# Optimization experiments

Measured on AMD Instinct MI355X. Metric: run time of the kernel, lower is better.

Reference implementation:

```python
import jax, jax.numpy as jnp
import numpy as np

# ---- ATSSPostProcessor config ----
PRE_NMS_THRESH = 0.05
PRE_NMS_TOP_N  = 400      # k candidates per image (pre_nms_top_n)
NMS_THRESH     = 0.4
POST_TOP_N     = 100      # fpn_post_nms_top_n
MIN_SIZE       = 0.0
NUM_ANGLE_BINS = 90
BBOX_W         = (10.0, 10.0, 5.0, 5.0)   # box_coder xywh weights; angle is passthrough (argmax-90 deg)
N, C, H, W     = 4, 15, 256, 256           # A=1 anchor per location
STRIDE, ANCHOR_SIZE = 8.0, 64.0
MAXV = 16                                   # vertex buffer for quad-quad clipping


def setup_inputs():
    key = jax.random.key(0)
    k1, k2, k3, k4 = jax.random.split(key, 4)
    box_cls = jax.random.normal(k1, (N, C, H, W), jnp.float32) - 2.0  # sigmoid ~0.12 avg -> plenty of candidates
    box_regression = jax.random.normal(k2, (N, 4, H, W), jnp.float32) * 0.5
    centerness = jax.random.normal(k3, (N, 1, H, W), jnp.float32)
    angle = jax.random.normal(k4, (N, NUM_ANGLE_BINS, H, W), jnp.float32)
    # xywha anchors on the stride-8 grid, row-major (H, W) to match permute_and_flatten ordering
    ys, xs = jnp.meshgrid(jnp.arange(H, dtype=jnp.float32), jnp.arange(W, dtype=jnp.float32), indexing='ij')
    cx = (xs.reshape(-1) + 0.5) * STRIDE
    cy = (ys.reshape(-1) + 0.5) * STRIDE
    wh = jnp.full((H * W,), ANCHOR_SIZE, jnp.float32)
    a0 = jnp.zeros((H * W,), jnp.float32)
    anchors = jnp.broadcast_to(jnp.stack([cx, cy, wh, wh, a0], -1), (N, H * W, 5))
    return {"box_cls": box_cls, "box_regression": box_regression, "centerness": centerness,
            "angle": angle, "anchors": jnp.asarray(anchors)}


def xywha_to_corners(b):
    # b [..., 5] (cx,cy,w,h,angle_deg) -> [..., 4, 2], CCW order
    cx, cy, w, h, a = b[..., 0], b[..., 1], b[..., 2], b[..., 3], b[..., 4]
    t = a * (jnp.pi / 180.0)
    c, s = jnp.cos(t), jnp.sin(t)
    ox = jnp.asarray([1., -1., -1., 1.], b.dtype) * (w[..., None] * 0.5)
    oy = jnp.asarray([1., 1., -1., -1.], b.dtype) * (h[..., None] * 0.5)
    x = cx[..., None] + ox * c[..., None] - oy * s[..., None]
    y = cy[..., None] + ox * s[..., None] + oy * c[..., None]
    return jnp.stack([x, y], -1)


def _clip_edge(poly, n, p1, p2):
    # Sutherland-Hodgman: clip CCW polygon (poly[:n]) against half-plane left of p1->p2
    e = p2 - p1
    d = e[0] * (poly[:, 1] - p1[1]) - e[1] * (poly[:, 0] - p1[0])  # >= 0 is inside
    def body(i, carry):
        out, m = carry
        j = jnp.where(i == n - 1, 0, i + 1)
        cur, nxt, dc, dn = poly[i], poly[j], d[i], d[j]
        denom = dc - dn
        denom = jnp.where(jnp.abs(denom) < 1e-8, 1e-8, denom)
        ip = cur + (dc / denom) * (nxt - cur)
        act = i < n
        a1 = act & (dc >= 0)
        out = out.at[m].set(jnp.where(a1, cur, out[m]))
        m = m + a1.astype(jnp.int32)
        a2 = act & ((dc >= 0) != (dn >= 0))
        out = out.at[m].set(jnp.where(a2, ip, out[m]))
        m = m + a2.astype(jnp.int32)
        return out, m
    return jax.lax.fori_loop(0, 8, body, (jnp.zeros_like(poly), jnp.int32(0)))


def _quad_inter_area(c1, c2):
    # intersection area of two CCW quads via polygon clipping + shoelace
    poly = jnp.zeros((MAXV, 2), c1.dtype).at[:4].set(c1)
    n = jnp.int32(4)
    def edge(e, carry):
        poly, n = carry
        return _clip_edge(poly, n, c2[e], c2[(e + 1) % 4])
    poly, n = jax.lax.fori_loop(0, 4, edge, (poly, n))
    idx = jnp.arange(MAXV)
    j = jnp.where(idx == n - 1, 0, idx + 1)
    mask = idx < n
    terms = poly[:, 0] * poly[j, 1] - poly[j, 0] * poly[:, 1]
    return 0.5 * jnp.abs(jnp.sum(jnp.where(mask, terms, 0.0)))


def _riou_matrix(boxes):                        # [k,5] -> [k,k] rotated IoU
    corners = xywha_to_corners(boxes)           # [k,4,2]
    areas = boxes[:, 2] * boxes[:, 3]
    def one(ci, ai):
        def two(cj, aj):
            inter = _quad_inter_area(ci, cj)
            return inter / (ai + aj - inter + 1e-7)
        return jax.vmap(two)(corners, areas)
    return jax.vmap(one)(corners, areas)


@jax.jit
def _forward(box_cls, box_regression, centerness, angle, anchors):
    n, c, h, w = box_cls.shape
    K, k = h * w, PRE_NMS_TOP_N
    # permute_and_flatten + activations
    cls = jax.nn.sigmoid(box_cls).transpose(0, 2, 3, 1).reshape(n, K, c)
    reg = box_regression.transpose(0, 2, 3, 1).reshape(n, K, 4)
    ctr = jax.nn.sigmoid(centerness).reshape(n, K)
    ang = jax.nn.softmax(angle.transpose(0, 2, 3, 1).reshape(n, K, NUM_ANGLE_BINS), axis=-1)
    # pre-nms threshold on raw sigmoid cls, topk on cls*centerness
    cand = cls > PRE_NMS_THRESH
    comb = cls * ctr[:, :, None]
    flat = jnp.where(cand, comb, -1.0).reshape(n, K * c)
    topv, topi = jax.lax.top_k(flat, k)          # sorted descending
    valid = topv > 0.0                           # emulates per_pre_nms_top_n clamp
    loc = topi // c
    labels = topi % c + 1
    reg_s = jnp.take_along_axis(reg, loc[..., None], axis=1)       # [n,k,4]
    anc_s = jnp.take_along_axis(anchors, loc[..., None], axis=1)   # [n,k,5]
    ang_s = jnp.take_along_axis(ang, loc[..., None], axis=1)       # [n,k,90]
    pred_angle = jnp.argmax(ang_s, axis=-1).astype(reg_s.dtype) - 90.0
    # box_coder.decode (xywh deltas, angle passthrough)
    wx, wy, ww, wh = BBOX_W
    dx, dy = reg_s[..., 0] / wx, reg_s[..., 1] / wy
    dw = jnp.clip(reg_s[..., 2] / ww, -10.0, 4.0)
    dh = jnp.clip(reg_s[..., 3] / wh, -10.0, 4.0)
    acx, acy, aw, ah = anc_s[..., 0], anc_s[..., 1], anc_s[..., 2], anc_s[..., 3]
    boxes = jnp.stack([dx * aw + acx, dy * ah + acy,
                       aw * jnp.exp(dw), ah * jnp.exp(dh), pred_angle], -1)
    valid = valid & (boxes[..., 2] >= MIN_SIZE) & (boxes[..., 3] >= MIN_SIZE)
    scores = jnp.where(valid, jnp.sqrt(jnp.maximum(topv, 0.0)), 0.0)
    # class-aware rotated NMS (boxlist_ml_rnms): IoU only within same class
    iou = jax.lax.stop_gradient(jax.vmap(_riou_matrix)(boxes))     # [n,k,k]
    same = labels[:, :, None] == labels[:, None, :]
    iou = jnp.where(same, iou, 0.0)
    idxs = jnp.arange(k)
    def body(i, keep):
        sup = keep[:, i][:, None] & (iou[:, i, :] > NMS_THRESH) & (idxs[None, :] > i)
        return keep & ~sup
    keep = jax.lax.fori_loop(0, k, body, valid)
    # keep top fpn_post_nms_top_n by score
    fscore = jnp.where(keep, scores, -1.0)
    fv, fi = jax.lax.top_k(fscore, POST_TOP_N)
    fvalid = fv > 0.0
    fboxes = jnp.take_along_axis(boxes, fi[..., None], axis=1)
    flabels = jnp.take_along_axis(labels, fi, axis=1)
    corners = xywha_to_corners(fboxes).reshape(n, POST_TOP_N, 8)   # convert('xyxyxyxy')
    out = jnp.concatenate([corners,
                           jnp.maximum(fv, 0.0)[..., None],
                           flabels.astype(corners.dtype)[..., None],
                           fvalid.astype(corners.dtype)[..., None]], -1)
    return out * fvalid[..., None].astype(out.dtype)   # [N, POST_TOP_N, 11]


def reference(box_cls, box_regression, centerness, angle, anchors):
    return _forward(box_cls, box_regression, centerness, angle, anchors)
```

## Files before the change

kernel.cpp:

```cpp
#include <hip/hip_runtime.h>
#include <math.h>

#define NIMG 4
#define NCLS 15
#define HW 65536
#define NANG 90
#define KTOP 400
#define POSTN 100
#define NBINS 4096
#define CAP 4096
#define SCAP 49152
#define SBUF 512
#define FLOOR_BIN 1434

#define HIST_OFF   0
#define SCNT_OFF   65536
#define SFLAG_OFF  65552
#define ZERO_BYTES 65600
#define SUPT_OFF   65600
#define STAGE_OFF  165952
#define SKEY_OFF   1738816
#define COR_OFF    1751616
#define AREA_OFF   1802816
#define LAB_OFF    1809216
#define SC_OFF     1815616
#define VAL_OFF    1822016
#define CCX_OFF    1828416
#define CCY_OFF    1834816
#define CRAD_OFF   1841216

__device__ __forceinline__ float sigmoidf(float x) {
    return 1.0f / (1.0f + expf(-x));
}

__global__ __launch_bounds__(256)
void k_hist(const float* __restrict__ cls, const float* __restrict__ ctr,
            int* __restrict__ hist, int* __restrict__ scnt,
            unsigned long long* __restrict__ stage, int* __restrict__ sflag) {
    __shared__ int sh[NBINS];
    __shared__ unsigned long long sbuf[SBUF];
    __shared__ int scount, sbase;
    const int n = blockIdx.y;
    const int p2 = (blockIdx.x * 256 + threadIdx.x) * 2;
    for (int b = threadIdx.x; b < NBINS; b += 256) sh[b] = 0;
    if (threadIdx.x == 0) scount = 0;
    __syncthreads();
    float2 cv2 = *(const float2*)(ctr + n * HW + p2);
    float cv[2] = {sigmoidf(cv2.x), sigmoidf(cv2.y)};
    for (int j = 0; j < NCLS; ++j) {
        float2 s2 = *(const float2*)(cls + (size_t)(n * NCLS + j) * HW + p2);
        float sv[2] = {s2.x, s2.y};
#pragma unroll
        for (int e = 0; e < 2; ++e) {
            float s = sigmoidf(sv[e]);
            if (s > 0.05f) {
                float comb = s * cv[e];
                int b = (int)(comb * 4096.0f);
                b = b < 0 ? 0 : (b > NBINS - 1 ? NBINS - 1 : b);
                atomicAdd(&sh[b], 1);
                if (b >= FLOOR_BIN) {
                    int m = atomicAdd(&scount, 1);
                    if (m < SBUF) {
                        unsigned int fb  = __float_as_uint(comb);
                        unsigned int idx = (unsigned int)((p2 + e) * NCLS + j);
                        sbuf[m] = ((unsigned long long)fb << 32) |
                                  (unsigned long long)(~idx);
                    }
                }
            }
        }
    }
    __syncthreads();
    for (int b = threadIdx.x; b < NBINS; b += 256) {
        int v = sh[b];
        if (v) atomicAdd(&hist[n * NBINS + b], v);
    }
    if (threadIdx.x == 0) {
        int c = scount;
        if (c > SBUF) { atomicOr(sflag, 1); c = SBUF; }
        sbase = atomicAdd(&scnt[n], c);
    }
    __syncthreads();
    int c = scount < SBUF ? scount : SBUF;
    int base = sbase;
    for (int m = threadIdx.x; m < c; m += 256) {
        int g = base + m;
        if (g < SCAP) stage[n * SCAP + g] = sbuf[m];
    }
}

__global__ __launch_bounds__(256)
void k_selstage(const unsigned long long* __restrict__ stage, const int* __restrict__ scnt,
                const int* __restrict__ sflag, const int* __restrict__ hist,
                const float* __restrict__ cls, const float* __restrict__ ctr,
                unsigned long long* __restrict__ skey) {
    const int n = blockIdx.x;
    __shared__ unsigned long long key[CAP];
    __shared__ int part[256];
    __shared__ int s_t, s_c;
    const int* hb = hist + n * NBINS;
    {
        int s = 0;
        int base = threadIdx.x * 16;
        for (int b = 0; b < 16; ++b) s += hb[base + b];
        part[threadIdx.x] = s;
        if (threadIdx.x == 0) { s_t = 0; s_c = 0; }
        __syncthreads();
        for (int off = 1; off < 256; off <<= 1) {
            int v = part[threadIdx.x] +
                    ((threadIdx.x + off < 256) ? part[threadIdx.x + off] : 0);
            __syncthreads();
            part[threadIdx.x] = v;
            __syncthreads();
        }
        int sg = threadIdx.x;
        int suf = part[sg];
        int above = (sg == 255) ? 0 : part[sg + 1];
        if (suf >= KTOP && above < KTOP) {
            int a2 = above, t = sg * 16;
            for (int b = sg * 16 + 15; b >= sg * 16; --b) {
                a2 += hb[b];
                if (a2 >= KTOP) { t = b; break; }
            }
            s_t = t;
        }
        __syncthreads();
    }
    const int t = s_t;
    const bool fb = (sflag[0] != 0) || (scnt[n] > SCAP) || (t < FLOOR_BIN);
    if (!fb) {
        const int sc = scnt[n];
        for (int m = threadIdx.x; m < sc; m += 256) {
            unsigned long long kk = stage[n * SCAP + m];
            float comb = __uint_as_float((unsigned int)(kk >> 32));
            int b = (int)(comb * 4096.0f);
            b = b < 0 ? 0 : (b > NBINS - 1 ? NBINS - 1 : b);
            if (b >= t) {
                int pos = atomicAdd(&s_c, 1);
                if (pos < CAP) key[pos] = kk;
            }
        }
    } else {
        for (int j = 0; j < NCLS; ++j) {
            for (int pos = threadIdx.x; pos < HW; pos += 256) {
                float s = sigmoidf(cls[(size_t)(n * NCLS + j) * HW + pos]);
                if (s > 0.05f) {
                    float comb = s * sigmoidf(ctr[n * HW + pos]);
                    int b = (int)(comb * 4096.0f);
                    b = b < 0 ? 0 : (b > NBINS - 1 ? NBINS - 1 : b);
                    if (b >= t) {
                        int p = atomicAdd(&s_c, 1);
                        if (p < CAP) {
                            unsigned int fbits = __float_as_uint(comb);
                            unsigned int idx = (unsigned int)(pos * NCLS + j);
                            key[p] = ((unsigned long long)fbits << 32) |
                                     (unsigned long long)(~idx);
                        }
                    }
                }
            }
        }
    }
    __syncthreads();
    int c = s_c;
    if (c > CAP) c = CAP;
    int S = 512;
    while (S < c) S <<= 1;
    for (int i = threadIdx.x; i < S; i += 256)
        if (i >= c) key[i] = 0ULL;
    __syncthreads();
    for (int k = 2; k <= S; k <<= 1) {
        for (int j = k >> 1; j > 0; j >>= 1) {
            for (int i = threadIdx.x; i < S; i += 256) {
                int l = i ^ j;
                if (l > i) {
                    unsigned long long a = key[i], b = key[l];
                    bool up = ((i & k) == 0);
                    if ((a > b) == up) { key[i] = b; key[l] = a; }
                }
            }
            __syncthreads();
        }
    }
    for (int r = threadIdx.x; r < KTOP; r += 256)
        skey[n * KTOP + r] = key[S - 1 - r];
}

__global__ __launch_bounds__(64)
void k_decode(const unsigned long long* __restrict__ skey,
              const float* __restrict__ reg, const float* __restrict__ ang,
              const float* __restrict__ anchors,
              float* __restrict__ cor, float* __restrict__ area, int* __restrict__ lab,
              float* __restrict__ sc, int* __restrict__ val,
              float* __restrict__ ccx, float* __restrict__ ccy, float* __restrict__ crad,
              unsigned long long* __restrict__ supT) {
#pragma clang fp contract(off)
    const int r = blockIdx.x;
    const int n = blockIdx.y;
    const int l = threadIdx.x;
    {
        int bid = n * KTOP + r;
        int z = bid * 8 + l;
        if (l < 8 && z < 12544) supT[z] = 0ULL;
    }
    const int base = n * KTOP + r;
    unsigned long long kk = skey[base];
    if (kk == 0ULL) {
        if (l == 0) {
            val[base] = 0; sc[base] = 0.0f; lab[base] = 0; area[base] = 0.0f;
            ccx[base] = 0.0f; ccy[base] = 0.0f; crad[base] = 0.0f;
            for (int q = 0; q < 8; ++q) cor[base * 8 + q] = 0.0f;
        }
        return;
    }
    unsigned int idx = ~((unsigned int)kk);
    int loc = (int)(idx / 15u);
    const float* ap = ang + ((size_t)n * NANG) * HW + loc;
    float bv = -INFINITY; int bb = 1000;
    for (int b = l; b < NANG; b += 64) {
        float v = ap[(size_t)b * HW];
        if (v > bv) { bv = v; bb = b; }
    }
    for (int off = 32; off > 0; off >>= 1) {
        float ov = __shfl_down(bv, off);
        int   ob = __shfl_down(bb, off);
        if (ov > bv || (ov == bv && ob < bb)) { bv = ov; bb = ob; }
    }
    if (l == 0) {
        int cl = (int)(idx % 15u);
        float topv = __uint_as_float((unsigned int)(kk >> 32));
        const float* rp = reg + ((size_t)n * 4) * HW + loc;
        float dx = rp[0] / 10.0f;
        float dy = rp[HW] / 10.0f;
        float dw = rp[2 * (size_t)HW] / 5.0f;
        float dh = rp[3 * (size_t)HW] / 5.0f;
        dw = fminf(fmaxf(dw, -10.0f), 4.0f);
        dh = fminf(fmaxf(dh, -10.0f), 4.0f);
        const float* an = anchors + ((size_t)n * HW + loc) * 5;
        float acx = an[0], acy = an[1], aw = an[2], ah = an[3];
        float bcx = dx * aw + acx;
        float bcy = dy * ah + acy;
        float bw = aw * expf(dw);
        float bh = ah * expf(dh);
        float pa = (float)bb - 90.0f;
        float th = pa * (float)0.017453292519943295;
        float cth = cosf(th), sth = sinf(th);
        float hw2 = bw * 0.5f, hh2 = bh * 0.5f;
        const float oxs[4] = {1.0f, -1.0f, -1.0f, 1.0f};
        const float oys[4] = {1.0f, 1.0f, -1.0f, -1.0f};
        for (int q = 0; q < 4; ++q) {
            float ox = oxs[q] * hw2, oy = oys[q] * hh2;
            cor[base * 8 + 2 * q]     = bcx + ox * cth - oy * sth;
            cor[base * 8 + 2 * q + 1] = bcy + ox * sth + oy * cth;
        }
        val[base] = 1;
        sc[base] = sqrtf(topv);
        lab[base] = cl + 1;
        area[base] = bw * bh;
        ccx[base] = bcx; ccy[base] = bcy;
        crad[base] = 0.5f * sqrtf(bw * bw + bh * bh);
    }
}

__device__ __forceinline__ float arr_get8(const float* a, int idx) {
    float r = a[0];
#pragma unroll
    for (int s = 1; s < 8; ++s) r = (s == idx) ? a[s] : r;
    return r;
}
__device__ __forceinline__ void arr_set8(float* a, int idx, float v) {
#pragma unroll
    for (int s = 0; s < 8; ++s) a[s] = (s == idx) ? v : a[s];
}

__device__ float quad_inter_area(const float* c1x, const float* c1y,
                                 const float* c2x, const float* c2y) {
#pragma clang fp contract(off)
    float px[8], py[8], qx[8], qy[8];
    int n = 4;
#pragma unroll
    for (int i = 0; i < 8; ++i) { px[i] = (i < 4) ? c1x[i] : 0.0f;
                                  py[i] = (i < 4) ? c1y[i] : 0.0f;
                                  qx[i] = 0.0f; qy[i] = 0.0f; }
#pragma unroll
    for (int e = 0; e < 4; ++e) {
        float p1x = c2x[e], p1y = c2y[e];
        int e2 = (e + 1) & 3;
        float ex = c2x[e2] - p1x, ey = c2y[e2] - p1y;
        int m = 0;
#pragma unroll
        for (int i = 0; i < 8; ++i) {
            if (i < n) {
                int j = (i == n - 1) ? 0 : i + 1;
                float cxi = px[i], cyi = py[i];
                float cxj = arr_get8(px, j), cyj = arr_get8(py, j);
                float dc = ex * (cyi - p1y) - ey * (cxi - p1x);
                float dn = ex * (cyj - p1y) - ey * (cxj - p1x);
                bool ic = (dc >= 0.0f), in2 = (dn >= 0.0f);
                if (ic) { arr_set8(qx, m, cxi); arr_set8(qy, m, cyi); ++m; }
                if (ic != in2) {
                    float denom = dc - dn;
                    if (fabsf(denom) < 1e-8f) denom = 1e-8f;
                    float tp = dc / denom;
                    arr_set8(qx, m, cxi + tp * (cxj - cxi));
                    arr_set8(qy, m, cyi + tp * (cyj - cyi));
                    ++m;
                }
            }
        }
        n = m;
        if (n == 0) return 0.0f;
#pragma unroll
        for (int i = 0; i < 8; ++i) { px[i] = qx[i]; py[i] = qy[i]; }
    }
    float ssum = 0.0f;
#pragma unroll
    for (int i = 0; i < 8; ++i) {
        if (i < n) {
            int j = (i == n - 1) ? 0 : i + 1;
            ssum += px[i] * arr_get8(py, j) - arr_get8(px, j) * py[i];
        }
    }
    return 0.5f * fabsf(ssum);
}

__global__ __launch_bounds__(256)
void k_pairs(const float* __restrict__ cor, const float* __restrict__ area,
             const int* __restrict__ lab,
             const float* __restrict__ ccx, const float* __restrict__ ccy,
             const float* __restrict__ crad,
             unsigned long long* __restrict__ supT) {
#pragma clang fp contract(off)
    const int n = blockIdx.y;
    const int p = blockIdx.x * 256 + threadIdx.x;
    if (p >= KTOP * KTOP) return;
    const int i = p / KTOP;
    const int j = p - i * KTOP;
    if (j <= i) return;
    const int base = n * KTOP;
    const int li = lab[base + i];
    if (li == 0 || lab[base + j] != li) return;
    float dx = ccx[base + i] - ccx[base + j];
    float dy = ccy[base + i] - ccy[base + j];
    float rr = crad[base + i] + crad[base + j];
    if (dx * dx + dy * dy > rr * rr) return;
    float cix[4], ciy[4], cjx[4], cjy[4];
    for (int q = 0; q < 4; ++q) {
        cix[q] = cor[(base + i) * 8 + 2 * q]; ciy[q] = cor[(base + i) * 8 + 2 * q + 1];
        cjx[q] = cor[(base + j) * 8 + 2 * q]; cjy[q] = cor[(base + j) * 8 + 2 * q + 1];
    }
    float inter = quad_inter_area(cix, ciy, cjx, cjy);
    float iou = inter / (area[base + i] + area[base + j] - inter + 1e-7f);
    if (iou > 0.4f) {
        atomicOr(&supT[((size_t)(n * 7 + (j >> 6)) * 7 + (i >> 6)) * 64 + (j & 63)],
                 1ULL << (i & 63));
    }
}

__global__ __launch_bounds__(64)
void k_nms_out(const unsigned long long* __restrict__ supT,
               const int* __restrict__ val,
               const float* __restrict__ cor, const float* __restrict__ sc,
               const int* __restrict__ lab, float* __restrict__ out) {
    const int n = blockIdx.x;
    const int l = threadIdx.x;
    unsigned removed = 0;
#pragma unroll
    for (int t = 0; t < 7; ++t) {
        int r = 64 * t + l;
        int v = (r < KTOP) ? val[n * KTOP + r] : 0;
        if (!v) removed |= (1u << t);
    }
    unsigned long long cm[7][7];
#pragma unroll
    for (int t = 0; t < 7; ++t)
#pragma unroll
        for (int rb = 0; rb < 7; ++rb)
            cm[t][rb] = supT[((size_t)(n * 7 + t) * 7 + rb) * 64 + l];
#pragma unroll
    for (int rb = 0; rb < 7; ++rb) {
        const int lim = (rb == 6) ? (KTOP - 384) : 64;
        for (int ib = 0; ib < lim; ++ib) {
            unsigned rm = (unsigned)__builtin_amdgcn_readlane((int)removed, ib);
            if (!((rm >> rb) & 1u)) {
                removed |= ((unsigned)((cm[0][rb] >> ib) & 1ULL));
                removed |= ((unsigned)((cm[1][rb] >> ib) & 1ULL)) << 1;
                removed |= ((unsigned)((cm[2][rb] >> ib) & 1ULL)) << 2;
                removed |= ((unsigned)((cm[3][rb] >> ib) & 1ULL)) << 3;
                removed |= ((unsigned)((cm[4][rb] >> ib) & 1ULL)) << 4;
                removed |= ((unsigned)((cm[5][rb] >> ib) & 1ULL)) << 5;
                removed |= ((unsigned)((cm[6][rb] >> ib) & 1ULL)) << 6;
            }
        }
    }
    __shared__ int order[POSTN];
    int rank = 0;
#pragma unroll
    for (int t = 0; t < 7; ++t) {
        bool kb = !((removed >> t) & 1u) && (64 * t + l < KTOP);
        unsigned long long m = __ballot(kb);
        int my = rank + __popcll(m & ((1ULL << l) - 1ULL));
        if (kb && my < POSTN) order[my] = 64 * t + l;
        rank += __popcll(m);
    }
    int kcnt = rank < POSTN ? rank : POSTN;
    __syncthreads();
    for (int e = l; e < POSTN * 11; e += 64) {
        int r = e / 11, c = e - r * 11;
        float v = 0.0f;
        if (r < kcnt) {
            int i = order[r];
            int b = n * KTOP + i;
            if (c < 8)       v = cor[b * 8 + c];
            else if (c == 8) v = sc[b];
            else if (c == 9) v = (float)lab[b];
            else             v = 1.0f;
        }
        out[(n * POSTN + r) * 11 + c] = v;
    }
}

extern "C" void kernel_launch(void* const* d_in, const int* in_sizes, int n_in,
                              void* d_out, int out_size, void* d_ws, size_t ws_size,
                              hipStream_t stream) {
    const float* box_cls = (const float*)d_in[0];
    const float* box_reg = (const float*)d_in[1];
    const float* ctr     = (const float*)d_in[2];
    const float* ang     = (const float*)d_in[3];
    const float* anchors = (const float*)d_in[4];
    float* out = (float*)d_out;
    char* ws = (char*)d_ws;

    int* hist  = (int*)(ws + HIST_OFF);
    int* scnt  = (int*)(ws + SCNT_OFF);
    int* sflag = (int*)(ws + SFLAG_OFF);
    unsigned long long* supT  = (unsigned long long*)(ws + SUPT_OFF);
    unsigned long long* stage = (unsigned long long*)(ws + STAGE_OFF);
    unsigned long long* skey  = (unsigned long long*)(ws + SKEY_OFF);
    float* cor  = (float*)(ws + COR_OFF);
    float* area = (float*)(ws + AREA_OFF);
    int* lab    = (int*)(ws + LAB_OFF);
    float* sc   = (float*)(ws + SC_OFF);
    int* val    = (int*)(ws + VAL_OFF);
    float* ccx  = (float*)(ws + CCX_OFF);
    float* ccy  = (float*)(ws + CCY_OFF);
    float* crad = (float*)(ws + CRAD_OFF);

    hipMemsetAsync(d_ws, 0, ZERO_BYTES, stream);
    k_hist    <<<dim3(HW / 512, NIMG), 256, 0, stream>>>(box_cls, ctr, hist,
                                                         scnt, stage, sflag);
    k_selstage<<<NIMG, 256, 0, stream>>>(stage, scnt, sflag, hist,
                                         box_cls, ctr, skey);
    k_decode  <<<dim3(KTOP, NIMG), 64, 0, stream>>>(skey, box_reg, ang, anchors,
                                                    cor, area, lab, sc, val,
                                                    ccx, ccy, crad, supT);
    k_pairs   <<<dim3((KTOP * KTOP + 255) / 256, NIMG), 256, 0, stream>>>(
                  cor, area, lab, ccx, ccy, crad, supT);
    k_nms_out <<<NIMG, 64, 0, stream>>>(supT, val, cor, sc, lab, out);
}
```

Measured before the change: 248.4 us.

## Drop memset and global histogram; fuse pair IoU with NMS in one block per image

The global histogram and atomics are removed from k_hist. Each block now writes its floor-passing candidates to a fixed per-block stage slot, and k_selstage builds the histogram in shared memory from the staged keys. The memset is gone. k_pairs and k_nms_out are merged into one 512-thread block per image that keeps the suppression mask in shared memory, which removes two launches and the global atomics. The trade-off is that all pairwise rotated-IoU work now runs on only 4 blocks, so parallelism drops sharply and the heavy polygon clipping may become the bottleneck.

```diff
diff --git a/kernel.cpp b/kernel.cpp
--- a/kernel.cpp
+++ b/kernel.cpp
@@ -9,25 +9,21 @@
 #define POSTN 100
 #define NBINS 4096
 #define CAP 4096
-#define SCAP 49152
+#define NBLK 128
 #define SBUF 512
-#define FLOOR_BIN 1434
-
-#define HIST_OFF   0
-#define SCNT_OFF   65536
-#define SFLAG_OFF  65552
-#define ZERO_BYTES 65600
-#define SUPT_OFF   65600
-#define STAGE_OFF  165952
-#define SKEY_OFF   1738816
-#define COR_OFF    1751616
-#define AREA_OFF   1802816
-#define LAB_OFF    1809216
-#define SC_OFF     1815616
-#define VAL_OFF    1822016
-#define CCX_OFF    1828416
-#define CCY_OFF    1834816
-#define CRAD_OFF   1841216
+#define FLOOR_VAL (1434.0f / 4096.0f)
+
+#define CNTB_OFF   0
+#define SKEY_OFF   2048
+#define COR_OFF    14848
+#define AREA_OFF   66048
+#define LAB_OFF    72448
+#define SC_OFF     78848
+#define VAL_OFF    85248
+#define CCX_OFF    91648
+#define CCY_OFF    98048
+#define CRAD_OFF   104448
+#define STAGE_OFF  110848
 
 __device__ __forceinline__ float sigmoidf(float x) {
     return 1.0f / (1.0f + expf(-x));
@@ -35,14 +31,12 @@
 
 __global__ __launch_bounds__(256)
 void k_hist(const float* __restrict__ cls, const float* __restrict__ ctr,
-            int* __restrict__ hist, int* __restrict__ scnt,
-            unsigned long long* __restrict__ stage, int* __restrict__ sflag) {
-    __shared__ int sh[NBINS];
+            int* __restrict__ cnt_blk, unsigned long long* __restrict__ stage) {
     __shared__ unsigned long long sbuf[SBUF];
-    __shared__ int scount, sbase;
+    __shared__ int scount;
     const int n = blockIdx.y;
-    const int p2 = (blockIdx.x * 256 + threadIdx.x) * 2;
-    for (int b = threadIdx.x; b < NBINS; b += 256) sh[b] = 0;
+    const int bx = blockIdx.x;
+    const int p2 = (bx * 256 + threadIdx.x) * 2;
     if (threadIdx.x == 0) scount = 0;
     __syncthreads();
     float2 cv2 = *(const float2*)(ctr + n * HW + p2);
@@ -53,73 +47,95 @@
 #pragma unroll
         for (int e = 0; e < 2; ++e) {
             float s = sigmoidf(sv[e]);
-            if (s > 0.05f) {
-                float comb = s * cv[e];
-                int b = (int)(comb * 4096.0f);
-                b = b < 0 ? 0 : (b > NBINS - 1 ? NBINS - 1 : b);
-                atomicAdd(&sh[b], 1);
-                if (b >= FLOOR_BIN) {
-                    int m = atomicAdd(&scount, 1);
-                    if (m < SBUF) {
-                        unsigned int fb  = __float_as_uint(comb);
-                        unsigned int idx = (unsigned int)((p2 + e) * NCLS + j);
-                        sbuf[m] = ((unsigned long long)fb << 32) |
-                                  (unsigned long long)(~idx);
-                    }
-                }
-            }
-        }
-    }
-    __syncthreads();
-    for (int b = threadIdx.x; b < NBINS; b += 256) {
-        int v = sh[b];
-        if (v) atomicAdd(&hist[n * NBINS + b], v);
-    }
-    if (threadIdx.x == 0) {
-        int c = scount;
-        if (c > SBUF) { atomicOr(sflag, 1); c = SBUF; }
-        sbase = atomicAdd(&scnt[n], c);
-    }
-    __syncthreads();
-    int c = scount < SBUF ? scount : SBUF;
-    int base = sbase;
-    for (int m = threadIdx.x; m < c; m += 256) {
-        int g = base + m;
-        if (g < SCAP) stage[n * SCAP + g] = sbuf[m];
-    }
+            float comb = s * cv[e];
+            if (comb >= FLOOR_VAL) {
+                int m = atomicAdd(&scount, 1);
+                if (m < SBUF) {
+                    unsigned int fb  = __float_as_uint(comb);
+                    unsigned int idx = (unsigned int)((p2 + e) * NCLS + j);
+                    sbuf[m] = ((unsigned long long)fb << 32) |
+                              (unsigned long long)(~idx);
+                }
+            }
+        }
+    }
+    __syncthreads();
+    int c = scount;
+    int cc = c > SBUF ? SBUF : c;
+    if (threadIdx.x == 0)
+        cnt_blk[n * NBLK + bx] = (c > SBUF) ? (cc | (1 << 31)) : cc;
+    unsigned long long* rp = stage + (size_t)(n * NBLK + bx) * SBUF;
+    for (int m = threadIdx.x; m < cc; m += 256) rp[m] = sbuf[m];
 }
 
 __global__ __launch_bounds__(256)
-void k_selstage(const unsigned long long* __restrict__ stage, const int* __restrict__ scnt,
-                const int* __restrict__ sflag, const int* __restrict__ hist,
+void k_selstage(const unsigned long long* __restrict__ stage,
+                const int* __restrict__ cnt_blk,
                 const float* __restrict__ cls, const float* __restrict__ ctr,
                 unsigned long long* __restrict__ skey) {
     const int n = blockIdx.x;
     __shared__ unsigned long long key[CAP];
+    __shared__ int hist[NBINS];
+    __shared__ int cbc[NBLK];
     __shared__ int part[256];
-    __shared__ int s_t, s_c;
-    const int* hb = hist + n * NBINS;
+    __shared__ int s_t, s_c, s_tot, s_ovf;
+    const int tid = threadIdx.x;
+    if (tid == 0) { s_t = 0; s_c = 0; s_tot = 0; s_ovf = 0; }
+    for (int b = tid; b < NBINS; b += 256) hist[b] = 0;
+    __syncthreads();
+    if (tid < NBLK) {
+        int v = cnt_blk[n * NBLK + tid];
+        int c = v & 0x7fffffff;
+        cbc[tid] = c;
+        atomicAdd(&s_tot, c);
+        if (v < 0) atomicOr(&s_ovf, 1);
+    }
+    __syncthreads();
+    const int r  = tid >> 1;
+    const int m0 = tid & 1;
+    const bool fb = (s_ovf != 0) || (s_tot < KTOP);
+    if (!fb) {
+        const unsigned long long* rp = stage + (size_t)(n * NBLK + r) * SBUF;
+        const int c = cbc[r];
+        for (int m = m0; m < c; m += 2) {
+            float comb = __uint_as_float((unsigned int)(rp[m] >> 32));
+            int b = (int)(comb * 4096.0f);
+            b = b < 0 ? 0 : (b > NBINS - 1 ? NBINS - 1 : b);
+            atomicAdd(&hist[b], 1);
+        }
+    } else {
+        for (int j = 0; j < NCLS; ++j) {
+            for (int pos = tid; pos < HW; pos += 256) {
+                float s = sigmoidf(cls[(size_t)(n * NCLS + j) * HW + pos]);
+                if (s > 0.05f) {
+                    float comb = s * sigmoidf(ctr[n * HW + pos]);
+                    int b = (int)(comb * 4096.0f);
+                    b = b < 0 ? 0 : (b > NBINS - 1 ? NBINS - 1 : b);
+                    atomicAdd(&hist[b], 1);
+                }
+            }
+        }
+    }
+    __syncthreads();
     {
         int s = 0;
-        int base = threadIdx.x * 16;
-        for (int b = 0; b < 16; ++b) s += hb[base + b];
-        part[threadIdx.x] = s;
-        if (threadIdx.x == 0) { s_t = 0; s_c = 0; }
+        int base = tid * 16;
+        for (int b = 0; b < 16; ++b) s += hist[base + b];
+        part[tid] = s;
         __syncthreads();
         for (int off = 1; off < 256; off <<= 1) {
-            int v = part[threadIdx.x] +
-                    ((threadIdx.x + off < 256) ? part[threadIdx.x + off] : 0);
+            int v = part[tid] + ((tid + off < 256) ? part[tid + off] : 0);
             __syncthreads();
-            part[threadIdx.x] = v;
+            part[tid] = v;
             __syncthreads();
         }
-        int sg = threadIdx.x;
+        int sg = tid;
         int suf = part[sg];
         int above = (sg == 255) ? 0 : part[sg + 1];
         if (suf >= KTOP && above < KTOP) {
             int a2 = above, t = sg * 16;
             for (int b = sg * 16 + 15; b >= sg * 16; --b) {
-                a2 += hb[b];
+                a2 += hist[b];
                 if (a2 >= KTOP) { t = b; break; }
             }
             s_t = t;
@@ -127,11 +143,11 @@
         __syncthreads();
     }
     const int t = s_t;
-    const bool fb = (sflag[0] != 0) || (scnt[n] > SCAP) || (t < FLOOR_BIN);
     if (!fb) {
-        const int sc = scnt[n];
-        for (int m = threadIdx.x; m < sc; m += 256) {
-            unsigned long long kk = stage[n * SCAP + m];
+        const unsigned long long* rp = stage + (size_t)(n * NBLK + r) * SBUF;
+        const int c = cbc[r];
+        for (int m = m0; m < c; m += 2) {
+            unsigned long long kk = rp[m];
             float comb = __uint_as_float((unsigned int)(kk >> 32));
             int b = (int)(comb * 4096.0f);
             b = b < 0 ? 0 : (b > NBINS - 1 ? NBINS - 1 : b);
@@ -142,19 +158,19 @@
         }
     } else {
         for (int j = 0; j < NCLS; ++j) {
-            for (int pos = threadIdx.x; pos < HW; pos += 256) {
+            for (int pos = tid; pos < HW; pos += 256) {
                 float s = sigmoidf(cls[(size_t)(n * NCLS + j) * HW + pos]);
                 if (s > 0.05f) {
                     float comb = s * sigmoidf(ctr[n * HW + pos]);
                     int b = (int)(comb * 4096.0f);
                     b = b < 0 ? 0 : (b > NBINS - 1 ? NBINS - 1 : b);
                     if (b >= t) {
-                        int p = atomicAdd(&s_c, 1);
-                        if (p < CAP) {
+                        int pos2 = atomicAdd(&s_c, 1);
+                        if (pos2 < CAP) {
                             unsigned int fbits = __float_as_uint(comb);
                             unsigned int idx = (unsigned int)(pos * NCLS + j);
-                            key[p] = ((unsigned long long)fbits << 32) |
-                                     (unsigned long long)(~idx);
+                            key[pos2] = ((unsigned long long)fbits << 32) |
+                                        (unsigned long long)(~idx);
                         }
                     }
                 }
@@ -166,12 +182,12 @@
     if (c > CAP) c = CAP;
     int S = 512;
     while (S < c) S <<= 1;
-    for (int i = threadIdx.x; i < S; i += 256)
+    for (int i = tid; i < S; i += 256)
         if (i >= c) key[i] = 0ULL;
     __syncthreads();
     for (int k = 2; k <= S; k <<= 1) {
         for (int j = k >> 1; j > 0; j >>= 1) {
-            for (int i = threadIdx.x; i < S; i += 256) {
+            for (int i = tid; i < S; i += 256) {
                 int l = i ^ j;
                 if (l > i) {
                     unsigned long long a = key[i], b = key[l];
@@ -182,8 +198,8 @@
             __syncthreads();
         }
     }
-    for (int r = threadIdx.x; r < KTOP; r += 256)
-        skey[n * KTOP + r] = key[S - 1 - r];
+    for (int r2 = tid; r2 < KTOP; r2 += 256)
+        skey[n * KTOP + r2] = key[S - 1 - r2];
 }
 
 __global__ __launch_bounds__(64)
@@ -192,17 +208,11 @@
               const float* __restrict__ anchors,
               float* __restrict__ cor, float* __restrict__ area, int* __restrict__ lab,
               float* __restrict__ sc, int* __restrict__ val,
-              float* __restrict__ ccx, float* __restrict__ ccy, float* __restrict__ crad,
-              unsigned long long* __restrict__ supT) {
+              float* __restrict__ ccx, float* __restrict__ ccy, float* __restrict__ crad) {
 #pragma clang fp contract(off)
     const int r = blockIdx.x;
     const int n = blockIdx.y;
     const int l = threadIdx.x;
-    {
-        int bid = n * KTOP + r;
-        int z = bid * 8 + l;
-        if (l < 8 && z < 12544) supT[z] = 0ULL;
-    }
     const int base = n * KTOP + r;
     unsigned long long kk = skey[base];
     if (kk == 0ULL) {
@@ -324,99 +334,111 @@
     return 0.5f * fabsf(ssum);
 }
 
-__global__ __launch_bounds__(256)
-void k_pairs(const float* __restrict__ cor, const float* __restrict__ area,
-             const int* __restrict__ lab,
-             const float* __restrict__ ccx, const float* __restrict__ ccy,
-             const float* __restrict__ crad,
-             unsigned long long* __restrict__ supT) {
+__global__ __launch_bounds__(512)
+void k_pairnms(const float* __restrict__ cor, const float* __restrict__ area,
+               const int* __restrict__ lab,
+               const float* __restrict__ ccx, const float* __restrict__ ccy,
+               const float* __restrict__ crad,
+               const int* __restrict__ val, const float* __restrict__ sc,
+               float* __restrict__ out) {
 #pragma clang fp contract(off)
-    const int n = blockIdx.y;
-    const int p = blockIdx.x * 256 + threadIdx.x;
-    if (p >= KTOP * KTOP) return;
-    const int i = p / KTOP;
-    const int j = p - i * KTOP;
-    if (j <= i) return;
+    const int n = blockIdx.x;
+    const int tid = threadIdx.x;
+    __shared__ unsigned int supL[7 * 7 * 64];
+    __shared__ unsigned int supH[7 * 7 * 64];
+    __shared__ int order[POSTN];
+    for (int z = tid; z < 7 * 7 * 64; z += 512) { supL[z] = 0u; supH[z] = 0u; }
+    __syncthreads();
     const int base = n * KTOP;
-    const int li = lab[base + i];
-    if (li == 0 || lab[base + j] != li) return;
-    float dx = ccx[base + i] - ccx[base + j];
-    float dy = ccy[base + i] - ccy[base + j];
-    float rr = crad[base + i] + crad[base + j];
-    if (dx * dx + dy * dy > rr * rr) return;
-    float cix[4], ciy[4], cjx[4], cjy[4];
-    for (int q = 0; q < 4; ++q) {
-        cix[q] = cor[(base + i) * 8 + 2 * q]; ciy[q] = cor[(base + i) * 8 + 2 * q + 1];
-        cjx[q] = cor[(base + j) * 8 + 2 * q]; cjy[q] = cor[(base + j) * 8 + 2 * q + 1];
-    }
-    float inter = quad_inter_area(cix, ciy, cjx, cjy);
-    float iou = inter / (area[base + i] + area[base + j] - inter + 1e-7f);
-    if (iou > 0.4f) {
-        atomicOr(&supT[((size_t)(n * 7 + (j >> 6)) * 7 + (i >> 6)) * 64 + (j & 63)],
-                 1ULL << (i & 63));
-    }
-}
-
-__global__ __launch_bounds__(64)
-void k_nms_out(const unsigned long long* __restrict__ supT,
-               const int* __restrict__ val,
-               const float* __restrict__ cor, const float* __restrict__ sc,
-               const int* __restrict__ lab, float* __restrict__ out) {
-    const int n = blockIdx.x;
-    const int l = threadIdx.x;
-    unsigned removed = 0;
-#pragma unroll
-    for (int t = 0; t < 7; ++t) {
-        int r = 64 * t + l;
-        int v = (r < KTOP) ? val[n * KTOP + r] : 0;
-        if (!v) removed |= (1u << t);
-    }
-    unsigned long long cm[7][7];
-#pragma unroll
-    for (int t = 0; t < 7; ++t)
-#pragma unroll
-        for (int rb = 0; rb < 7; ++rb)
-            cm[t][rb] = supT[((size_t)(n * 7 + t) * 7 + rb) * 64 + l];
-#pragma unroll
-    for (int rb = 0; rb < 7; ++rb) {
-        const int lim = (rb == 6) ? (KTOP - 384) : 64;
-        for (int ib = 0; ib < lim; ++ib) {
-            unsigned rm = (unsigned)__builtin_amdgcn_readlane((int)removed, ib);
-            if (!((rm >> rb) & 1u)) {
-                removed |= ((unsigned)((cm[0][rb] >> ib) & 1ULL));
-                removed |= ((unsigned)((cm[1][rb] >> ib) & 1ULL)) << 1;
-                removed |= ((unsigned)((cm[2][rb] >> ib) & 1ULL)) << 2;
-                removed |= ((unsigned)((cm[3][rb] >> ib) & 1ULL)) << 3;
-                removed |= ((unsigned)((cm[4][rb] >> ib) & 1ULL)) << 4;
-                removed |= ((unsigned)((cm[5][rb] >> ib) & 1ULL)) << 5;
-                removed |= ((unsigned)((cm[6][rb] >> ib) & 1ULL)) << 6;
-            }
-        }
-    }
-    __shared__ int order[POSTN];
-    int rank = 0;
-#pragma unroll
-    for (int t = 0; t < 7; ++t) {
-        bool kb = !((removed >> t) & 1u) && (64 * t + l < KTOP);
-        unsigned long long m = __ballot(kb);
-        int my = rank + __popcll(m & ((1ULL << l) - 1ULL));
-        if (kb && my < POSTN) order[my] = 64 * t + l;
-        rank += __popcll(m);
-    }
-    int kcnt = rank < POSTN ? rank : POSTN;
-    __syncthreads();
-    for (int e = l; e < POSTN * 11; e += 64) {
-        int r = e / 11, c = e - r * 11;
-        float v = 0.0f;
-        if (r < kcnt) {
-            int i = order[r];
-            int b = n * KTOP + i;
-            if (c < 8)       v = cor[b * 8 + c];
-            else if (c == 8) v = sc[b];
-            else if (c == 9) v = (float)lab[b];
-            else             v = 1.0f;
-        }
-        out[(n * POSTN + r) * 11 + c] = v;
+    const int wid = tid >> 6, lane = tid & 63;
+    for (int i = wid; i < KTOP; i += 8) {
+        const int li = lab[base + i];
+        if (li != 0) {
+            const float xi = ccx[base + i], yi = ccy[base + i];
+            const float ri = crad[base + i], ai = area[base + i];
+            float cix[4], ciy[4];
+            for (int q = 0; q < 4; ++q) {
+                cix[q] = cor[(base + i) * 8 + 2 * q];
+                ciy[q] = cor[(base + i) * 8 + 2 * q + 1];
+            }
+            for (int j = i + 1 + lane; j < KTOP; j += 64) {
+                if (lab[base + j] != li) continue;
+                float dx = xi - ccx[base + j];
+                float dy = yi - ccy[base + j];
+                float rr = ri + crad[base + j];
+                if (dx * dx + dy * dy > rr * rr) continue;
+                float cjx[4], cjy[4];
+                for (int q = 0; q < 4; ++q) {
+                    cjx[q] = cor[(base + j) * 8 + 2 * q];
+                    cjy[q] = cor[(base + j) * 8 + 2 * q + 1];
+                }
+                float inter = quad_inter_area(cix, ciy, cjx, cjy);
+                float iou = inter / (ai + area[base + j] - inter + 1e-7f);
+                if (iou > 0.4f) {
+                    int sidx = ((j >> 6) * 7 + (i >> 6)) * 64 + (j & 63);
+                    if ((i & 63) < 32) atomicOr(&supL[sidx], 1u << (i & 31));
+                    else               atomicOr(&supH[sidx], 1u << (i & 31));
+                }
+            }
+        }
+    }
+    __syncthreads();
+    if (tid < 64) {
+        const int l = tid;
+        unsigned removed = 0;
+#pragma unroll
+        for (int t = 0; t < 7; ++t) {
+            int r = 64 * t + l;
+            int v = (r < KTOP) ? val[base + r] : 0;
+            if (!v) removed |= (1u << t);
+        }
+#pragma unroll
+        for (int rb = 0; rb < 7; ++rb) {
+            unsigned long long cmr[7];
+#pragma unroll
+            for (int t = 0; t < 7; ++t) {
+                int sidx = (t * 7 + rb) * 64 + l;
+                cmr[t] = ((unsigned long long)supH[sidx] << 32) |
+                         (unsigned long long)supL[sidx];
+            }
+            const int lim = (rb == 6) ? (KTOP - 384) : 64;
+            for (int ib = 0; ib < lim; ++ib) {
+                unsigned rm = (unsigned)__builtin_amdgcn_readlane((int)removed, ib);
+                if (!((rm >> rb) & 1u)) {
+                    removed |= ((unsigned)((cmr[0] >> ib) & 1ULL));
+                    removed |= ((unsigned)((cmr[1] >> ib) & 1ULL)) << 1;
+                    removed |= ((unsigned)((cmr[2] >> ib) & 1ULL)) << 2;
+                    removed |= ((unsigned)((cmr[3] >> ib) & 1ULL)) << 3;
+                    removed |= ((unsigned)((cmr[4] >> ib) & 1ULL)) << 4;
+                    removed |= ((unsigned)((cmr[5] >> ib) & 1ULL)) << 5;
+                    removed |= ((unsigned)((cmr[6] >> ib) & 1ULL)) << 6;
+                }
+            }
+        }
+        int rank = 0;
+#pragma unroll
+        for (int t = 0; t < 7; ++t) {
+            bool kb = !((removed >> t) & 1u) && (64 * t + l < KTOP);
+            unsigned long long m = __ballot(kb);
+            int my = rank + __popcll(m & ((1ULL << l) - 1ULL));
+            if (kb && my < POSTN) order[my] = 64 * t + l;
+            rank += __popcll(m);
+        }
+        int kcnt = rank < POSTN ? rank : POSTN;
+        __threadfence_block();
+        for (int e = l; e < POSTN * 11; e += 64) {
+            int r = e / 11, c = e - r * 11;
+            float v = 0.0f;
+            if (r < kcnt) {
+                int i = order[r];
+                int b = base + i;
+                if (c < 8)       v = cor[b * 8 + c];
+                else if (c == 8) v = sc[b];
+                else if (c == 9) v = (float)lab[b];
+                else             v = 1.0f;
+            }
+            out[(n * POSTN + r) * 11 + c] = v;
+        }
     }
 }
 
@@ -431,12 +453,9 @@
     float* out = (float*)d_out;
     char* ws = (char*)d_ws;
 
-    int* hist  = (int*)(ws + HIST_OFF);
-    int* scnt  = (int*)(ws + SCNT_OFF);
-    int* sflag = (int*)(ws + SFLAG_OFF);
-    unsigned long long* supT  = (unsigned long long*)(ws + SUPT_OFF);
+    int* cnt_blk = (int*)(ws + CNTB_OFF);
+    unsigned long long* skey  = (unsigned long long*)(ws + SKEY_OFF);
     unsigned long long* stage = (unsigned long long*)(ws + STAGE_OFF);
-    unsigned long long* skey  = (unsigned long long*)(ws + SKEY_OFF);
     float* cor  = (float*)(ws + COR_OFF);
     float* area = (float*)(ws + AREA_OFF);
     int* lab    = (int*)(ws + LAB_OFF);
@@ -446,15 +465,11 @@
     float* ccy  = (float*)(ws + CCY_OFF);
     float* crad = (float*)(ws + CRAD_OFF);
 
-    hipMemsetAsync(d_ws, 0, ZERO_BYTES, stream);
-    k_hist    <<<dim3(HW / 512, NIMG), 256, 0, stream>>>(box_cls, ctr, hist,
-                                                         scnt, stage, sflag);
-    k_selstage<<<NIMG, 256, 0, stream>>>(stage, scnt, sflag, hist,
-                                         box_cls, ctr, skey);
+    k_hist    <<<dim3(NBLK, NIMG), 256, 0, stream>>>(box_cls, ctr, cnt_blk, stage);
+    k_selstage<<<NIMG, 256, 0, stream>>>(stage, cnt_blk, box_cls, ctr, skey);
     k_decode  <<<dim3(KTOP, NIMG), 64, 0, stream>>>(skey, box_reg, ang, anchors,
                                                     cor, area, lab, sc, val,
-                                                    ccx, ccy, crad, supT);
-    k_pairs   <<<dim3((KTOP * KTOP + 255) / 256, NIMG), 256, 0, stream>>>(
-                  cor, area, lab, ccx, ccy, crad, supT);
-    k_nms_out <<<NIMG, 64, 0, stream>>>(supT, val, cor, sc, lab, out);
-}
+                                                    ccx, ccy, crad);
+    k_pairnms <<<NIMG, 512, 0, stream>>>(cor, area, lab, ccx, ccy, crad,
+                                         val, sc, out);
+}
```

New measurement: 314.7 us. 26.7% more time.
